# Optimization experiments

Measured on AMD Instinct MI355X. Metric: run time of the kernel, lower is better.

The kernel has to match this reference:

```python
import jax, jax.numpy as jnp
import numpy as np
from functools import partial

B, N, D = 32, 256, 1024
H = 16
HD = D // H
CD = 1024          # cond_dim
E = 4              # num_experts
TOPK = 2
DFF = 4 * D        # expert hidden
RH = 2 * D         # router mlp hidden
TEMP = 1.0
EPS = 1e-5


def _ln(x, g, b):
    mu = jnp.mean(x, axis=-1, keepdims=True)
    var = jnp.var(x, axis=-1, keepdims=True)
    return (x - mu) * jax.lax.rsqrt(var + EPS) * g + b


def setup_inputs() -> dict:
    key = jax.random.key(0)
    ks = jax.random.split(key, 16)
    s = 0.02
    return {
        "x": jax.random.normal(ks[0], (B, N, D), jnp.float32),
        "cond": jax.random.normal(ks[1], (B, 1, CD), jnp.float32),
        "ln1_g": jnp.ones((D,), jnp.float32),
        "ln1_b": jnp.zeros((D,), jnp.float32),
        "qkv_w": jax.random.normal(ks[2], (D, 3 * D), jnp.float32) * s,
        "proj_w": jax.random.normal(ks[3], (D, D), jnp.float32) * s,
        "proj_b": jnp.zeros((D,), jnp.float32),
        "ln2_g": jnp.ones((D,), jnp.float32),
        "ln2_b": jnp.zeros((D,), jnp.float32),
        "r_fc1_w": jax.random.normal(ks[4], (D + CD, RH), jnp.float32) * s,
        "r_fc1_b": jnp.zeros((RH,), jnp.float32),
        "r_fc2_w": jax.random.normal(ks[5], (RH, E), jnp.float32) * s,
        "r_fc2_b": jnp.zeros((E,), jnp.float32),
        "e_w1": jax.random.normal(ks[6], (E, D, DFF), jnp.float32) * s,
        "e_b1": jnp.zeros((E, DFF), jnp.float32),
        "e_w2": jax.random.normal(ks[7], (E, DFF, D), jnp.float32) * s,
        "e_b2": jnp.zeros((E, D), jnp.float32),
    }


def reference(x, cond, ln1_g, ln1_b, qkv_w, proj_w, proj_b, ln2_g, ln2_b,
              r_fc1_w, r_fc1_b, r_fc2_w, r_fc2_b, e_w1, e_b1, e_w2, e_b2):
    gelu = partial(jax.nn.gelu, approximate=False)  # torch nn.GELU default (erf)

    # ---- Attention block (pre-LN, no mask, qkv_bias=False) ----
    h = _ln(x, ln1_g, ln1_b)
    qkv = (h @ qkv_w).reshape(B, N, 3, H, HD)
    q, k, v = jnp.moveaxis(qkv, 2, 0)                         # each [B,N,H,HD]
    scale = HD ** -0.5
    attn = jnp.einsum("bqhd,bkhd->bhqk", q * scale, k)        # [B,H,N,N]
    attn = jax.nn.softmax(attn, axis=-1)
    o = jnp.einsum("bhqk,bkhd->bqhd", attn, v).reshape(B, N, D)
    x = x + o @ proj_w + proj_b

    # ---- RouterCond: concat tokens with repeated cond, MLP -> expert logits ----
    h = _ln(x, ln2_g, ln2_b)
    cond_rep = jnp.broadcast_to(cond, (B, N, CD))             # repeat along seq
    rin = jnp.concatenate([h, cond_rep], axis=-1).reshape(-1, D + CD)  # [T, D+CD]
    logits = gelu(rin @ r_fc1_w + r_fc1_b) @ r_fc2_w + r_fc2_b         # [T, E]
    logits = (logits - jnp.max(logits, axis=-1, keepdims=True)) / TEMP
    probs = jnp.clip(jax.nn.softmax(logits, axis=-1), 1e-9, 1.0 - 1e-9)

    # top-k selection + renormalization, scatter to dense router mask [T, E]
    top_p, top_i = jax.lax.top_k(probs, TOPK)
    top_w = top_p / jnp.sum(top_p, axis=-1, keepdims=True)    # normalize=True
    T = B * N
    router_mask = jnp.zeros((T, E), probs.dtype).at[
        jnp.arange(T)[:, None], top_i].set(top_w)             # [T, E]

    # ---- Expert MLPs, combined by router weights ----
    hf = h.reshape(T, D)
    hid = gelu(jnp.einsum("td,edh->teh", hf, e_w1) + e_b1)    # [T, E, DFF]
    eout = jnp.einsum("teh,ehd->ted", hid, e_w2) + e_b2       # [T, E, D]
    moe = jnp.einsum("te,ted->td", router_mask, eout).reshape(B, N, D)

    return x + moe
```

## Files before the change

kernel.cpp:

```cpp
#include <hip/hip_runtime.h>


typedef unsigned short u16;
typedef unsigned int   u32;

typedef __bf16 bf16x8 __attribute__((ext_vector_type(8)));
typedef float  floatx4 __attribute__((ext_vector_type(4)));

__device__ __forceinline__ float b2f(u32 u) {
    union { float f; u32 i; } v; v.i = (u & 0xffffu) << 16; return v.f;
}
__device__ __forceinline__ u16 f2b(float f) {
    union { float f; u32 i; } v; v.f = f;
    u32 x = v.i;
    u32 r = (x + 0x7fffu + ((x >> 16) & 1u)) >> 16;
    return (u16)r;
}
__device__ __forceinline__ float gelu_f(float x) {
    return 0.5f * x * (1.0f + erff(x * 0.70710678118654752440f));
}
__device__ __forceinline__ float lmix(const void* p, size_t i, int isf) {
    return isf ? ((const float*)p)[i] : b2f(((const u16*)p)[i]);
}
__device__ __forceinline__ void ld8(const void* p, size_t i, int isf, float w[8]) {
    if (isf) {
        const float* q = (const float*)p + i;
        float4 a = *(const float4*)q, b = *(const float4*)(q + 4);
        w[0] = a.x; w[1] = a.y; w[2] = a.z; w[3] = a.w;
        w[4] = b.x; w[5] = b.y; w[6] = b.z; w[7] = b.w;
    } else {
        const u16* q = (const u16*)p + i;
        uint4 r = *(const uint4*)q;
        w[0] = b2f(r.x); w[1] = b2f(r.x >> 16);
        w[2] = b2f(r.y); w[3] = b2f(r.y >> 16);
        w[4] = b2f(r.z); w[5] = b2f(r.z >> 16);
        w[6] = b2f(r.w); w[7] = b2f(r.w >> 16);
    }
}
__device__ __forceinline__ void ld4(const void* p, size_t i, int isf, float w[4]) {
    if (isf) {
        float4 a = *(const float4*)((const float*)p + i);
        w[0] = a.x; w[1] = a.y; w[2] = a.z; w[3] = a.w;
    } else {
        uint2 r = *(const uint2*)((const u16*)p + i);
        w[0] = b2f(r.x); w[1] = b2f(r.x >> 16);
        w[2] = b2f(r.y); w[3] = b2f(r.y >> 16);
    }
}

__global__ void init_kernel(const void* x0, int* cb) {
    __shared__ int sh[256];
    const int tid = threadIdx.x;
    if (tid < 12) cb[tid] = 0;
    int bad = 0;
    const u16* p = (const u16*)x0;
    for (int i = tid; i < 4096; i += 256) {
        float v = b2f(p[2 * i]);
        float a = fabsf(v);
        if (!(a <= 1e3f) || (v != 0.f && a < 1e-8f)) bad++;
    }
    sh[tid] = bad;
    __syncthreads();
    for (int s = 128; s > 0; s >>= 1) {
        if (tid < s) sh[tid] += sh[tid + s];
        __syncthreads();
    }
    if (tid == 0) cb[12] = (sh[0] > 512) ? 1 : 0;
}

__global__ __launch_bounds__(256) void cond_kernel(
    const void* __restrict__ cond, const void* __restrict__ w1,
    float* __restrict__ ct, const int* __restrict__ flg)
{
    const int isf = flg[12];
    const int b = blockIdx.y;
    const int col0 = blockIdx.x * 64;
    const int tid = threadIdx.x;
    const int wave = tid >> 6, lane = tid & 63;
    __shared__ float a[1024];
    __shared__ float part[4][64];
    {
        float v[4];
        ld4(cond, (size_t)b * 1024 + tid * 4, isf, v);
        a[tid * 4 + 0] = v[0]; a[tid * 4 + 1] = v[1];
        a[tid * 4 + 2] = v[2]; a[tid * 4 + 3] = v[3];
    }
    __syncthreads();
    const int col = col0 + lane;
    float s = 0.f;
    const int kbase = wave * 256;
    #pragma unroll 4
    for (int k = 0; k < 256; k++)
        s = fmaf(a[kbase + k], lmix(w1, (size_t)(1024 + kbase + k) * 2048 + col, isf), s);
    part[wave][lane] = s;
    __syncthreads();
    if (wave == 0) {
        float r = (part[0][lane] + part[1][lane]) + (part[2][lane] + part[3][lane]);
        ct[(size_t)b * 2048 + col] = r;
    }
}

__global__ __launch_bounds__(256) void pack_ln_kernel(
    int mode, const void* __restrict__ xin, size_t rowbase,
    const void* __restrict__ g, const void* __restrict__ bta,
    const float* __restrict__ mu_g, const float* __restrict__ rs_g,
    u16* __restrict__ hpk, u16* __restrict__ hb, const int* __restrict__ flg)
{
    const int isf = flg[12];
    const int row = blockIdx.x, tid = threadIdx.x;
    float v[4];
    float mu, rsv;
    __shared__ float red[8];
    __shared__ float mu_rs[2];
    if (mode == 0) {
        ld4(xin, (rowbase + row) * 1024 + tid * 4, isf, v);
        float s = v[0] + v[1] + v[2] + v[3];
        float q = v[0] * v[0] + v[1] * v[1] + v[2] * v[2] + v[3] * v[3];
        #pragma unroll
        for (int off = 32; off > 0; off >>= 1) {
            s += __shfl_down(s, off, 64);
            q += __shfl_down(q, off, 64);
        }
        int wid = tid >> 6, lane = tid & 63;
        if (lane == 0) { red[wid] = s; red[4 + wid] = q; }
        __syncthreads();
        if (tid == 0) {
            float ts = red[0] + red[1] + red[2] + red[3];
            float tq = red[4] + red[5] + red[6] + red[7];
            float m = ts * (1.0f / 1024.0f);
            float var = tq * (1.0f / 1024.0f) - m * m;
            float xx = var + 1e-5f;
            float r = rsqrtf(xx);
            r = r * (1.5f - 0.5f * xx * r * r);
            mu_rs[0] = m; mu_rs[1] = r;
        }
        __syncthreads();
        mu = mu_rs[0]; rsv = mu_rs[1];
    } else {
        float4 t = *(const float4*)((const float*)xin + (rowbase + row) * 1024 + tid * 4);
        v[0] = t.x; v[1] = t.y; v[2] = t.z; v[3] = t.w;
        mu = mu_g[rowbase + row]; rsv = rs_g[rowbase + row];
    }
    float gg[4], bb[4];
    ld4(g, tid * 4, isf, gg);
    ld4(bta, tid * 4, isf, bb);
    u16 hi[4], lo[4];
    #pragma unroll
    for (int i = 0; i < 4; i++) {
        float h = (v[i] - mu) * rsv * gg[i] + bb[i];
        hi[i] = f2b(h);
        lo[i] = f2b(h - b2f(hi[i]));
    }
    uint2 ph, pl;
    ph.x = (u32)hi[0] | ((u32)hi[1] << 16);
    ph.y = (u32)hi[2] | ((u32)hi[3] << 16);
    pl.x = (u32)lo[0] | ((u32)lo[1] << 16);
    pl.y = (u32)lo[2] | ((u32)lo[3] << 16);
    *(uint2*)(hpk + (size_t)row * 2048 + tid * 4) = ph;
    *(uint2*)(hpk + (size_t)row * 2048 + 1024 + tid * 4) = pl;
    if (hb) *(uint2*)(hb + (rowbase + row) * 1024 + tid * 4) = ph;
}

__global__ __launch_bounds__(256) void pack_wt_kernel(
    const void* __restrict__ W, int N, int K,
    u16* __restrict__ Bt, const int* __restrict__ flg)
{
    const int isf = flg[12];
    __shared__ float sh[64][65];
    const int k0 = blockIdx.x * 64, n0 = blockIdx.y * 64;
    const int tid = threadIdx.x;
    #pragma unroll
    for (int i = 0; i < 4; i++) {
        int r = (tid >> 4) + i * 16, c = (tid & 15) * 4;
        float w[4];
        ld4(W, (size_t)(k0 + r) * N + n0 + c, isf, w);
        sh[r][c] = w[0]; sh[r][c + 1] = w[1]; sh[r][c + 2] = w[2]; sh[r][c + 3] = w[3];
    }
    __syncthreads();
    const int n = tid >> 2, kc = (tid & 3) * 16;
    u16 hi[16], lo[16];
    #pragma unroll
    for (int j = 0; j < 16; j++) {
        float v = sh[kc + j][n];
        hi[j] = f2b(v);
        lo[j] = f2b(v - b2f(hi[j]));
    }
    u16* dst = Bt + (size_t)(n0 + n) * (2 * K) + k0 + kc;
    uint4 a, b;
    a.x = (u32)hi[0] | ((u32)hi[1] << 16);  a.y = (u32)hi[2] | ((u32)hi[3] << 16);
    a.z = (u32)hi[4] | ((u32)hi[5] << 16);  a.w = (u32)hi[6] | ((u32)hi[7] << 16);
    b.x = (u32)hi[8] | ((u32)hi[9] << 16);  b.y = (u32)hi[10] | ((u32)hi[11] << 16);
    b.z = (u32)hi[12] | ((u32)hi[13] << 16); b.w = (u32)hi[14] | ((u32)hi[15] << 16);
    *(uint4*)dst = a; *(uint4*)(dst + 8) = b;
    a.x = (u32)lo[0] | ((u32)lo[1] << 16);  a.y = (u32)lo[2] | ((u32)lo[3] << 16);
    a.z = (u32)lo[4] | ((u32)lo[5] << 16);  a.w = (u32)lo[6] | ((u32)lo[7] << 16);
    b.x = (u32)lo[8] | ((u32)lo[9] << 16);  b.y = (u32)lo[10] | ((u32)lo[11] << 16);
    b.z = (u32)lo[12] | ((u32)lo[13] << 16); b.w = (u32)lo[14] | ((u32)lo[15] << 16);
    *(uint4*)(dst + K) = a; *(uint4*)(dst + K + 8) = b;
}

__global__ __launch_bounds__(256) void pack_wtb_kernel(
    const void* __restrict__ W, size_t wOff, int N, int K,
    u16* __restrict__ Bt, const int* __restrict__ flg)
{
    const int isf = flg[12];
    __shared__ float sh[64][65];
    const int k0 = blockIdx.x * 64, n0 = blockIdx.y * 64;
    const int tid = threadIdx.x;
    #pragma unroll
    for (int i = 0; i < 4; i++) {
        int r = (tid >> 4) + i * 16, c = (tid & 15) * 4;
        float w[4];
        ld4(W, wOff + (size_t)(k0 + r) * N + n0 + c, isf, w);
        sh[r][c] = w[0]; sh[r][c + 1] = w[1]; sh[r][c + 2] = w[2]; sh[r][c + 3] = w[3];
    }
    __syncthreads();
    const int n = tid >> 2, kc = (tid & 3) * 16;
    u16 hi[16];
    #pragma unroll
    for (int j = 0; j < 16; j++) hi[j] = f2b(sh[kc + j][n]);
    u16* dst = Bt + (size_t)(n0 + n) * K + k0 + kc;
    uint4 a, b;
    a.x = (u32)hi[0] | ((u32)hi[1] << 16);  a.y = (u32)hi[2] | ((u32)hi[3] << 16);
    a.z = (u32)hi[4] | ((u32)hi[5] << 16);  a.w = (u32)hi[6] | ((u32)hi[7] << 16);
    b.x = (u32)hi[8] | ((u32)hi[9] << 16);  b.y = (u32)hi[10] | ((u32)hi[11] << 16);
    b.z = (u32)hi[12] | ((u32)hi[13] << 16); b.w = (u32)hi[14] | ((u32)hi[15] << 16);
    *(uint4*)dst = a; *(uint4*)(dst + 8) = b;
}

__global__ __launch_bounds__(256) void pack_sb_rows_kernel(
    const float* __restrict__ src, u16* __restrict__ dst)
{
    const int row = blockIdx.x, tid = threadIdx.x;
    float4 t = *(const float4*)(src + (size_t)row * 1024 + tid * 4);
    float v[4] = {t.x, t.y, t.z, t.w};
    u16 hi[4], lo[4];
    #pragma unroll
    for (int i = 0; i < 4; i++) {
        hi[i] = f2b(v[i]);
        lo[i] = f2b(v[i] - b2f(hi[i]));
    }
    uint2 ph, pl;
    ph.x = (u32)hi[0] | ((u32)hi[1] << 16);
    ph.y = (u32)hi[2] | ((u32)hi[3] << 16);
    pl.x = (u32)lo[0] | ((u32)lo[1] << 16);
    pl.y = (u32)lo[2] | ((u32)lo[3] << 16);
    *(uint2*)(dst + (size_t)row * 2048 + tid * 4) = ph;
    *(uint2*)(dst + (size_t)row * 2048 + 1024 + tid * 4) = pl;
}

#define SB_PLAIN 0
#define SB_FC1   1
#define SB_PROJ  2

__global__ __launch_bounds__(256) void gemm_sb(
    int mode,
    const u16* __restrict__ Ap,
    const u16* __restrict__ Bt,
    int K,
    float* __restrict__ C, int ldc,
    const void* __restrict__ bias,
    const float* __restrict__ condt,
    const void* __restrict__ resid,
    int rowbase, const int* __restrict__ flg)
{
    const int isf = flg[12];
    __shared__ __align__(16) u16 Ah[128][40];
    __shared__ __align__(16) u16 Al[128][40];
    __shared__ __align__(16) u16 Bh[128][40];
    __shared__ __align__(16) u16 Bl[128][40];
    const int tid = threadIdx.x;
    const int row0 = blockIdx.y * 128, col0 = blockIdx.x * 128;
    const int wave = tid >> 6, lane = tid & 63;
    const int wm = (wave >> 1) * 64, wn = (wave & 1) * 64;
    const int ln = lane & 15, quad = lane >> 4;
    const size_t K2 = (size_t)2 * K;
    floatx4 acc[4][4];
    #pragma unroll
    for (int i = 0; i < 4; i++)
        #pragma unroll
        for (int j = 0; j < 4; j++) acc[i][j] = (floatx4){0.f, 0.f, 0.f, 0.f};

    const int ar = tid >> 1, ac = (tid & 1) * 16;
    uint4 pa0, pa1, pal0, pal1, pb0, pb1, pbl0, pbl1;

    {
        const u16* ap = Ap + (size_t)(row0 + ar) * K2 + ac;
        pa0 = *(const uint4*)ap;        pa1 = *(const uint4*)(ap + 8);
        pal0 = *(const uint4*)(ap + K); pal1 = *(const uint4*)(ap + K + 8);
        const u16* bp = Bt + (size_t)(col0 + ar) * K2 + ac;
        pb0 = *(const uint4*)bp;        pb1 = *(const uint4*)(bp + 8);
        pbl0 = *(const uint4*)(bp + K); pbl1 = *(const uint4*)(bp + K + 8);
    }

    for (int k0 = 0; k0 < K; k0 += 32) {
        __syncthreads();
        *(uint4*)&Ah[ar][ac] = pa0;  *(uint4*)&Ah[ar][ac + 8] = pa1;
        *(uint4*)&Al[ar][ac] = pal0; *(uint4*)&Al[ar][ac + 8] = pal1;
        *(uint4*)&Bh[ar][ac] = pb0;  *(uint4*)&Bh[ar][ac + 8] = pb1;
        *(uint4*)&Bl[ar][ac] = pbl0; *(uint4*)&Bl[ar][ac + 8] = pbl1;
        __syncthreads();
        if (k0 + 32 < K) {
            const u16* ap = Ap + (size_t)(row0 + ar) * K2 + k0 + 32 + ac;
            pa0 = *(const uint4*)ap;        pa1 = *(const uint4*)(ap + 8);
            pal0 = *(const uint4*)(ap + K); pal1 = *(const uint4*)(ap + K + 8);
            const u16* bp = Bt + (size_t)(col0 + ar) * K2 + k0 + 32 + ac;
            pb0 = *(const uint4*)bp;        pb1 = *(const uint4*)(bp + 8);
            pbl0 = *(const uint4*)(bp + K); pbl1 = *(const uint4*)(bp + K + 8);
        }
        bf16x8 ah[4], al[4];
        #pragma unroll
        for (int mt = 0; mt < 4; mt++) {
            ah[mt] = *(const bf16x8*)&Ah[wm + mt * 16 + ln][quad * 8];
            al[mt] = *(const bf16x8*)&Al[wm + mt * 16 + ln][quad * 8];
        }
        #pragma unroll
        for (int nt = 0; nt < 4; nt++) {
            bf16x8 bh = *(const bf16x8*)&Bh[wn + nt * 16 + ln][quad * 8];
            bf16x8 bl = *(const bf16x8*)&Bl[wn + nt * 16 + ln][quad * 8];
            #pragma unroll
            for (int mt = 0; mt < 4; mt++) {
                acc[mt][nt] = __builtin_amdgcn_mfma_f32_16x16x32_bf16(ah[mt], bh, acc[mt][nt], 0, 0, 0);
                acc[mt][nt] = __builtin_amdgcn_mfma_f32_16x16x32_bf16(ah[mt], bl, acc[mt][nt], 0, 0, 0);
                acc[mt][nt] = __builtin_amdgcn_mfma_f32_16x16x32_bf16(al[mt], bh, acc[mt][nt], 0, 0, 0);
            }
        }
    }
    #pragma unroll
    for (int mt = 0; mt < 4; mt++) {
        #pragma unroll
        for (int nt = 0; nt < 4; nt++) {
            #pragma unroll
            for (int r = 0; r < 4; r++) {
                int row = row0 + wm + mt * 16 + quad * 4 + r;
                int col = col0 + wn + nt * 16 + ln;
                float v = acc[mt][nt][r];
                if (mode == SB_FC1)
                    v = gelu_f(v + lmix(bias, col, isf) +
                               condt[(size_t)((rowbase + row) >> 8) * 2048 + col]);
                else if (mode == SB_PROJ)
                    v += lmix(bias, col, isf) + lmix(resid, (size_t)row * ldc + col, isf);
                C[(size_t)row * ldc + col] = v;
            }
        }
    }
}

#define MOE_FC1 0
#define MOE_FC2 1

__global__ __launch_bounds__(256) void gemm_moe(
    int mode,
    const u16* __restrict__ Ap,
    const u16* __restrict__ Bt,
    int K,
    u16* __restrict__ C, int ldc,
    const void* __restrict__ bias, size_t biasOff,
    const float* __restrict__ rowscale,
    const int* __restrict__ toklist,
    const int* __restrict__ cb, int e, int rowOff,
    const int* __restrict__ flg)
{
    const int isf = flg[12];
    const int Meff = cb[e];
    const int gbase = cb[4 + e];
    const int rg0 = rowOff + blockIdx.y * 128;
    if (rg0 >= Meff) return;
    const int col0 = blockIdx.x * 128;
    __shared__ __align__(16) u16 As[128][40];
    __shared__ __align__(16) u16 Bs[128][40];
    const int tid = threadIdx.x;
    const int wave = tid >> 6, lane = tid & 63;
    const int wm = (wave >> 1) * 64, wn = (wave & 1) * 64;
    const int ln = lane & 15, quad = lane >> 4;
    floatx4 acc[4][4];
    #pragma unroll
    for (int i = 0; i < 4; i++)
        #pragma unroll
        for (int j = 0; j < 4; j++) acc[i][j] = (floatx4){0.f, 0.f, 0.f, 0.f};

    const int ar = tid >> 1, ac = (tid & 1) * 16;
    const int rg = rg0 + ar;
    const bool valid = (rg < Meff);
    const u16* arow;
    if (mode == MOE_FC1) {
        int tokid = valid ? toklist[gbase + rg] : 0;
        arow = Ap + (size_t)tokid * K;
    } else {
        arow = Ap + (size_t)(rg - rowOff) * K;
    }
    const u16* brow = Bt + (size_t)(col0 + ar) * K;
    uint4 pa0 = {0u,0u,0u,0u}, pa1 = {0u,0u,0u,0u}, pb0, pb1;
    if (valid) { pa0 = *(const uint4*)(arow + ac); pa1 = *(const uint4*)(arow + ac + 8); }
    pb0 = *(const uint4*)(brow + ac); pb1 = *(const uint4*)(brow + ac + 8);

    for (int k0 = 0; k0 < K; k0 += 32) {
        __syncthreads();
        *(uint4*)&As[ar][ac] = pa0; *(uint4*)&As[ar][ac + 8] = pa1;
        *(uint4*)&Bs[ar][ac] = pb0; *(uint4*)&Bs[ar][ac + 8] = pb1;
        __syncthreads();
        if (k0 + 32 < K) {
            if (valid) {
                pa0 = *(const uint4*)(arow + k0 + 32 + ac);
                pa1 = *(const uint4*)(arow + k0 + 32 + ac + 8);
            }
            pb0 = *(const uint4*)(brow + k0 + 32 + ac);
            pb1 = *(const uint4*)(brow + k0 + 32 + ac + 8);
        }
        bf16x8 a[4];
        #pragma unroll
        for (int mt = 0; mt < 4; mt++)
            a[mt] = *(const bf16x8*)&As[wm + mt * 16 + ln][quad * 8];
        #pragma unroll
        for (int nt = 0; nt < 4; nt++) {
            bf16x8 b = *(const bf16x8*)&Bs[wn + nt * 16 + ln][quad * 8];
            #pragma unroll
            for (int mt = 0; mt < 4; mt++)
                acc[mt][nt] = __builtin_amdgcn_mfma_f32_16x16x32_bf16(a[mt], b, acc[mt][nt], 0, 0, 0);
        }
    }
    #pragma unroll
    for (int mt = 0; mt < 4; mt++) {
        #pragma unroll
        for (int nt = 0; nt < 4; nt++) {
            #pragma unroll
            for (int r = 0; r < 4; r++) {
                int gw = rg0 + wm + mt * 16 + quad * 4 + r;
                if (gw >= Meff) continue;
                int col = col0 + wn + nt * 16 + ln;
                float v = acc[mt][nt][r] + lmix(bias, biasOff + col, isf);
                if (mode == MOE_FC1) {
                    C[(size_t)(gw - rowOff) * ldc + col] = f2b(gelu_f(v));
                } else {
                    v *= rowscale[gbase + gw];
                    C[(size_t)(gbase + gw) * ldc + col] = f2b(v);
                }
            }
        }
    }
}

__global__ __launch_bounds__(256) void gemm_moe2(
    const u16* __restrict__ Ap,
    const u16* __restrict__ Bt,
    u16* __restrict__ C,
    const void* __restrict__ bias, size_t biasOff,
    const float* __restrict__ rowscale,
    const int* __restrict__ cb, int e, int rowOff,
    const int* __restrict__ flg)
{
    const int isf = flg[12];
    const int Meff = cb[e];
    const int gbase = cb[4 + e];
    const int rg0 = rowOff + blockIdx.y * 128;
    if (rg0 >= Meff) return;
    const int col0 = blockIdx.x * 64;
    const int K = 4096;
    __shared__ __align__(16) u16 As[128][40];
    __shared__ __align__(16) u16 Bs[64][40];
    const int tid = threadIdx.x;
    const int wave = tid >> 6, lane = tid & 63;
    const int ln = lane & 15, quad = lane >> 4;
    floatx4 acc[2][4];
    #pragma unroll
    for (int i = 0; i < 2; i++)
        #pragma unroll
        for (int j = 0; j < 4; j++) acc[i][j] = (floatx4){0.f, 0.f, 0.f, 0.f};

    const int ar = tid >> 1, ac = (tid & 1) * 16;
    const int br = tid >> 2, bc = (tid & 3) * 8;
    const int rg = rg0 + ar;
    const bool valid = (rg < Meff);
    const u16* arow = Ap + (size_t)(rg - rowOff) * K;
    const u16* brow = Bt + (size_t)(col0 + br) * K;
    uint4 pa0 = {0u,0u,0u,0u}, pa1 = {0u,0u,0u,0u}, pb;
    if (valid) { pa0 = *(const uint4*)(arow + ac); pa1 = *(const uint4*)(arow + ac + 8); }
    pb = *(const uint4*)(brow + bc);

    for (int k0 = 0; k0 < K; k0 += 32) {
        __syncthreads();
        *(uint4*)&As[ar][ac] = pa0; *(uint4*)&As[ar][ac + 8] = pa1;
        *(uint4*)&Bs[br][bc] = pb;
        __syncthreads();
        if (k0 + 32 < K) {
            if (valid) {
                pa0 = *(const uint4*)(arow + k0 + 32 + ac);
                pa1 = *(const uint4*)(arow + k0 + 32 + ac + 8);
            }
            pb = *(const uint4*)(brow + k0 + 32 + bc);
        }
        bf16x8 a0 = *(const bf16x8*)&As[wave * 32 + ln][quad * 8];
        bf16x8 a1 = *(const bf16x8*)&As[wave * 32 + 16 + ln][quad * 8];
        #pragma unroll
        for (int nt = 0; nt < 4; nt++) {
            bf16x8 b = *(const bf16x8*)&Bs[nt * 16 + ln][quad * 8];
            acc[0][nt] = __builtin_amdgcn_mfma_f32_16x16x32_bf16(a0, b, acc[0][nt], 0, 0, 0);
            acc[1][nt] = __builtin_amdgcn_mfma_f32_16x16x32_bf16(a1, b, acc[1][nt], 0, 0, 0);
        }
// ... 364 lines not shown
    float* Ks = sh;
    float* Vs = sh + 64 * 68;

    const int q = qt * 64 + lane;
    float qreg[64];
    const float* qp = qkv + (size_t)(b * 256 + q) * 3072 + hh * 64;
    #pragma unroll
    for (int i = 0; i < 16; i++) *(float4*)&qreg[i * 4] = *(const float4*)(qp + i * 4);

    float oa[64];
    #pragma unroll
    for (int d = 0; d < 64; d++) oa[d] = 0.f;
    float m = -1e30f, l = 0.f;

    for (int s = 0; s < 4; s++) {
        __syncthreads();
        {
            int r = tid >> 2;
            int c = (tid & 3) * 16;
            int key = (r >> 4) * 64 + s * 16 + (r & 15);
            const float* kp = qkv + (size_t)(b * 256 + key) * 3072 + 1024 + hh * 64 + c;
            #pragma unroll
            for (int i = 0; i < 4; i++) {
                *(float4*)&Ks[r * 68 + c + i * 4] = *(const float4*)(kp + i * 4);
                *(float4*)&Vs[r * 68 + c + i * 4] = *(const float4*)(kp + 1024 + i * 4);
            }
        }
        __syncthreads();
        const float* Kw = Ks + wave * 16 * 68;
        const float* Vw = Vs + wave * 16 * 68;
        for (int jj = 0; jj < 16; jj++) {
            float s0 = 0.f, s1 = 0.f, s2 = 0.f, s3 = 0.f;
            #pragma unroll
            for (int d = 0; d < 64; d += 4) {
                s0 = fmaf(qreg[d + 0], Kw[jj * 68 + d + 0], s0);
                s1 = fmaf(qreg[d + 1], Kw[jj * 68 + d + 1], s1);
                s2 = fmaf(qreg[d + 2], Kw[jj * 68 + d + 2], s2);
                s3 = fmaf(qreg[d + 3], Kw[jj * 68 + d + 3], s3);
            }
            float sc = ((s0 + s1) + (s2 + s3)) * 0.125f;
            float mn = fmaxf(m, sc);
            float c = __expf(m - mn);
            float p = __expf(sc - mn);
            l = l * c + p;
            #pragma unroll
            for (int d = 0; d < 64; d++)
                oa[d] = fmaf(oa[d], c, p * Vw[jj * 68 + d]);
            m = mn;
        }
    }

    __syncthreads();
    if (wave == 1 || wave == 3) {
        float* dst = sh + (wave >> 1) * (64 * 66) + lane * 66;
        #pragma unroll
        for (int d = 0; d < 64; d++) dst[d] = oa[d];
        dst[64] = m; dst[65] = l;
    }
    __syncthreads();
    if (wave == 0 || wave == 2) {
        const float* src = sh + (wave >> 1) * (64 * 66) + lane * 66;
        float m2 = src[64], l2 = src[65];
        float M = fmaxf(m, m2);
        float c1 = __expf(m - M), c2 = __expf(m2 - M);
        l = l * c1 + l2 * c2;
        #pragma unroll
        for (int d = 0; d < 64; d++) oa[d] = oa[d] * c1 + src[d] * c2;
        m = M;
    }
    __syncthreads();
    if (wave == 2) {
        float* dst = sh + lane * 66;
        #pragma unroll
        for (int d = 0; d < 64; d++) dst[d] = oa[d];
        dst[64] = m; dst[65] = l;
    }
    __syncthreads();
    if (wave == 0) {
        const float* src = sh + lane * 66;
        float m2 = src[64], l2 = src[65];
        float M = fmaxf(m, m2);
        float c1 = __expf(m - M), c2 = __expf(m2 - M);
        l = l * c1 + l2 * c2;
        #pragma unroll
        for (int d = 0; d < 64; d++) oa[d] = oa[d] * c1 + src[d] * c2;
        float inv = 1.0f / l;
        float* op = o + (size_t)(b * 256 + q) * 1024 + hh * 64;
        #pragma unroll
        for (int i = 0; i < 16; i++) {
            float4 v = { oa[i * 4] * inv, oa[i * 4 + 1] * inv,
                         oa[i * 4 + 2] * inv, oa[i * 4 + 3] * inv };
            *(float4*)(op + i * 4) = v;
        }
    }
}

__global__ __launch_bounds__(256) void router_kernel(
    const float* __restrict__ hr, const void* __restrict__ w2,
    const void* __restrict__ b2, int* __restrict__ t2i,
    float* __restrict__ t2w, int* __restrict__ cb, int rowbase,
    const int* __restrict__ flg)
{
    const int isf = flg[12];
    const int lt = blockIdx.x * 4 + (threadIdx.x >> 6);
    const int t = rowbase + lt;
    const int lane = threadIdx.x & 63;
    float a0 = 0.f, a1 = 0.f, a2 = 0.f, a3 = 0.f;
    const float* hp = hr + (size_t)lt * 2048;
    #pragma unroll
    for (int it = 0; it < 8; it++) {
        const int j = it * 256 + lane * 4;
        float4 hv = *(const float4*)(hp + j);
        float w[4];
        ld4(w2, (size_t)(j + 0) * 4, isf, w);
        a0 = fmaf(hv.x, w[0], a0); a1 = fmaf(hv.x, w[1], a1);
        a2 = fmaf(hv.x, w[2], a2); a3 = fmaf(hv.x, w[3], a3);
        ld4(w2, (size_t)(j + 1) * 4, isf, w);
        a0 = fmaf(hv.y, w[0], a0); a1 = fmaf(hv.y, w[1], a1);
        a2 = fmaf(hv.y, w[2], a2); a3 = fmaf(hv.y, w[3], a3);
        ld4(w2, (size_t)(j + 2) * 4, isf, w);
        a0 = fmaf(hv.z, w[0], a0); a1 = fmaf(hv.z, w[1], a1);
        a2 = fmaf(hv.z, w[2], a2); a3 = fmaf(hv.z, w[3], a3);
        ld4(w2, (size_t)(j + 3) * 4, isf, w);
        a0 = fmaf(hv.w, w[0], a0); a1 = fmaf(hv.w, w[1], a1);
        a2 = fmaf(hv.w, w[2], a2); a3 = fmaf(hv.w, w[3], a3);
    }
    #pragma unroll
    for (int off = 32; off > 0; off >>= 1) {
        a0 += __shfl_down(a0, off, 64);
        a1 += __shfl_down(a1, off, 64);
        a2 += __shfl_down(a2, off, 64);
        a3 += __shfl_down(a3, off, 64);
    }
    if (lane == 0) {
        float l[4];
        l[0] = a0 + lmix(b2, 0, isf); l[1] = a1 + lmix(b2, 1, isf);
        l[2] = a2 + lmix(b2, 2, isf); l[3] = a3 + lmix(b2, 3, isf);
        int i0 = 0;
        #pragma unroll
        for (int i = 1; i < 4; i++) if (l[i] > l[i0]) i0 = i;
        int i1 = (i0 == 0) ? 1 : 0;
        #pragma unroll
        for (int i = 0; i < 4; i++) if (i != i0 && l[i] > l[i1]) i1 = i;
        float mx = fmaxf(fmaxf(l[0], l[1]), fmaxf(l[2], l[3]));
        float e0 = __expf(l[0] - mx), e1 = __expf(l[1] - mx);
        float e2 = __expf(l[2] - mx), e3 = __expf(l[3] - mx);
        float inv = 1.0f / (e0 + e1 + e2 + e3);
        float p[4] = { e0 * inv, e1 * inv, e2 * inv, e3 * inv };
        float b0 = fminf(fmaxf(p[i0], 1e-9f), 1.0f - 1e-9f);
        float b1 = fminf(fmaxf(p[i1], 1e-9f), 1.0f - 1e-9f);
        float winv = 1.0f / (b0 + b1);
        t2i[2 * t] = i0; t2i[2 * t + 1] = i1;
        t2w[2 * t] = b0 * winv; t2w[2 * t + 1] = b1 * winv;
        atomicAdd(&cb[i0], 1);
        atomicAdd(&cb[i1], 1);
    }
}

__global__ __launch_bounds__(256) void fill2_kernel(
    const int* __restrict__ t2i, const float* __restrict__ t2w,
    int* __restrict__ cb, int* __restrict__ tok,
    float* __restrict__ aw, int* __restrict__ apos)
{
    const int e = blockIdx.x;
    const int tid = threadIdx.x;
    __shared__ int scan[256];
    int base = 0;
    #pragma unroll
    for (int i = 0; i < 4; i++) if (i < e) base += cb[i];
    const int t0 = tid * 32;
    int cnt = 0;
    for (int t = t0; t < t0 + 32; t++)
        cnt += (t2i[2 * t] == e) + (t2i[2 * t + 1] == e);
    scan[tid] = cnt;
    __syncthreads();
    for (int off = 1; off < 256; off <<= 1) {
        int add = (tid >= off) ? scan[tid - off] : 0;
        __syncthreads();
        scan[tid] += add;
        __syncthreads();
    }
    int pos = base + scan[tid] - cnt;
    for (int t = t0; t < t0 + 32; t++) {
        #pragma unroll
        for (int j = 0; j < 2; j++) {
            if (t2i[2 * t + j] == e) {
                tok[pos] = t;
                aw[pos] = t2w[2 * t + j];
                apos[2 * t + j] = pos;
                pos++;
            }
        }
    }
    if (tid == 0) cb[4 + e] = base;
}

#define EM_FC1 0
#define EM_FC2 1

__global__ __launch_bounds__(256) void gemm_mfma(
    int mode,
    const float* __restrict__ x1,
    const float* __restrict__ mu, const float* __restrict__ rs,
    const void* __restrict__ lng, const void* __restrict__ lnb,
    const u16* __restrict__ Ab,
    const void* __restrict__ B, size_t bOff, int ldb, int K,
    u16* __restrict__ C, int ldc,
    const void* __restrict__ bias, size_t biasOff,
    const float* __restrict__ rowscale,
    const int* __restrict__ toklist,
    const int* __restrict__ cb, int e, int rowOff,
    const int* __restrict__ flg)
{
    const int isf = flg[12];
    const int Meff = cb[e];
    const int gbase = cb[4 + e];
    const int rg0 = rowOff + blockIdx.y * 64;
    if (rg0 >= Meff) return;
    const int col0 = blockIdx.x * 64;
    __shared__ __align__(16) u16 As[64][72];
    __shared__ __align__(16) u16 Bs[64][72];
    const int tid = threadIdx.x;
    const int wave = tid >> 6, lane = tid & 63;
    const int ln = lane & 15, quad = lane >> 4;
    floatx4 acc[4];
    #pragma unroll
    for (int nt = 0; nt < 4; nt++) acc[nt] = (floatx4){0.f, 0.f, 0.f, 0.f};

    const int ar = tid >> 2, ac = (tid & 3) * 8;
    const int bk = tid >> 3, bn = (tid & 7) * 8;
    const int rg = rg0 + ar;
    const bool valid = (rg < Meff);
    int tokid = 0; float lm = 0.f, lr = 0.f;
    if (mode == EM_FC1 && valid) {
        tokid = toklist[gbase + rg];
        lm = mu[tokid]; lr = rs[tokid];
    }

    for (int k0 = 0; k0 < K; k0 += 32) {
        __syncthreads();
        if (mode == EM_FC1) {
            uint4 packed = {0u, 0u, 0u, 0u};
            if (valid) {
                float4 p0 = *(const float4*)(x1 + (size_t)tokid * 1024 + k0 + ac);
                float4 p1 = *(const float4*)(x1 + (size_t)tokid * 1024 + k0 + ac + 4);
                float pv[8] = {p0.x, p0.y, p0.z, p0.w, p1.x, p1.y, p1.z, p1.w};
                float gg[8], bb[8];
                ld8(lng, k0 + ac, isf, gg);
                ld8(lnb, k0 + ac, isf, bb);
                u16 wb[8];
                #pragma unroll
                for (int z = 0; z < 8; z++)
                    wb[z] = f2b((pv[z] - lm) * lr * gg[z] + bb[z]);
                packed.x = (u32)wb[0] | ((u32)wb[1] << 16);
                packed.y = (u32)wb[2] | ((u32)wb[3] << 16);
                packed.z = (u32)wb[4] | ((u32)wb[5] << 16);
                packed.w = (u32)wb[6] | ((u32)wb[7] << 16);
            }
            *(uint4*)&As[ar][ac] = packed;
        } else {
            uint4 av = {0u, 0u, 0u, 0u};
            if (valid) av = *(const uint4*)(Ab + (size_t)(rg - rowOff) * K + k0 + ac);
            *(uint4*)&As[ar][ac] = av;
        }
        u16 u[8];
        {
            float w[8];
            ld8(B, bOff + (size_t)(k0 + bk) * ldb + col0 + bn, isf, w);
            #pragma unroll
            for (int z = 0; z < 8; z++) u[z] = f2b(w[z]);
        }
        #pragma unroll
        for (int jj = 0; jj < 8; jj++) {
            int j = (jj + (tid & 7)) & 7;
            Bs[bn + j][bk] = u[j];
        }
        __syncthreads();
        bf16x8 af = *(const bf16x8*)&As[wave * 16 + ln][quad * 8];
        #pragma unroll
        for (int nt = 0; nt < 4; nt++) {
            bf16x8 bf = *(const bf16x8*)&Bs[nt * 16 + ln][quad * 8];
            acc[nt] = __builtin_amdgcn_mfma_f32_16x16x32_bf16(af, bf, acc[nt], 0, 0, 0);
        }
    }
    #pragma unroll
    for (int nt = 0; nt < 4; nt++) {
        #pragma unroll
        for (int r = 0; r < 4; r++) {
            int gw = rg0 + wave * 16 + quad * 4 + r;
            if (gw >= Meff) continue;
            int gcol = col0 + nt * 16 + ln;
            float v = acc[nt][r] + lmix(bias, biasOff + gcol, isf);
            if (mode == EM_FC1) {
                C[(size_t)(gw - rowOff) * ldc + gcol] = f2b(gelu_f(v));
            } else {
                v *= rowscale[gbase + gw];
                C[(size_t)(gbase + gw) * ldc + gcol] = f2b(v);
            }
        }
    }
}

__global__ __launch_bounds__(256) void combine_kernel(
    const float* __restrict__ x1, const u16* __restrict__ eo,
    const int* __restrict__ apos, void* __restrict__ outv,
    const int* __restrict__ flg)
{
    const int isf = flg[12];
    int t = blockIdx.x;
    int c = threadIdx.x * 4;
    int p0 = apos[2 * t], p1 = apos[2 * t + 1];
    float4 xv = *(const float4*)(x1 + (size_t)t * 1024 + c);
    uint2 ea = *(const uint2*)(eo + (size_t)p0 * 1024 + c);
    uint2 eb = *(const uint2*)(eo + (size_t)p1 * 1024 + c);
    float r0 = xv.x + b2f(ea.x) + b2f(eb.x);
    float r1 = xv.y + b2f(ea.x >> 16) + b2f(eb.x >> 16);
    float r2 = xv.z + b2f(ea.y) + b2f(eb.y);
    float r3 = xv.w + b2f(ea.y >> 16) + b2f(eb.y >> 16);
    if (isf) {
        float4 res = {r0, r1, r2, r3};
        *(float4*)((float*)outv + (size_t)t * 1024 + c) = res;
    } else {
        uint2 res;
        res.x = (u32)f2b(r0) | ((u32)f2b(r1) << 16);
        res.y = (u32)f2b(r2) | ((u32)f2b(r3) << 16);
        *(uint2*)((u16*)outv + (size_t)t * 1024 + c) = res;
    }
}

extern "C" void kernel_launch(void* const* d_in, const int* in_sizes, int n_in,
                              void* d_out, int out_size, void* d_ws, size_t ws_size,
                              hipStream_t stream)
{
    const void* x      = d_in[0];
    const void* cond   = d_in[1];
    const void* ln1_g  = d_in[2];
    const void* ln1_b  = d_in[3];
    const void* qkv_w  = d_in[4];
    const void* proj_w = d_in[5];
    const void* proj_b = d_in[6];
    const void* ln2_g  = d_in[7];
    const void* ln2_b  = d_in[8];
    const void* rf1w   = d_in[9];
    const void* rf1b   = d_in[10];
    const void* rf2w   = d_in[11];
    const void* rf2b   = d_in[12];
    const void* ew1    = d_in[13];
    const void* eb1    = d_in[14];
    const void* ew2    = d_in[15];
    const void* eb2    = d_in[16];
    (void)in_sizes; (void)n_in; (void)out_size;

    char* ws = (char*)d_ws;
    const size_t MB = 1024 * 1024;
    const bool fat = ws_size >= (size_t)116 * MB;

    float* x1   = (float*)(ws);
    u16*   qkvt = (u16*)(ws);
    u16*   hpk  = (u16*)(ws + 12 * MB);
    float* qkvcFb = (float*)(ws + 16 * MB);
    char*  B1   = ws + 32 * MB;
    float* ob   = (float*)B1;
    u16*   rf1tF= (u16*)B1;
    u16*   h2tF = (u16*)(ws + 40 * MB);
    u16*   eo   = (u16*)B1;
    u16*   rf1tB= (u16*)B1;
    char*  R    = ws + 64 * MB;
    float* qkvcF= (float*)R;
    u16*   h2tB = (u16*)R;
    float* hrcB = (float*)(R + 8 * MB);
    float* hrcF = (float*)R;
    u16*   hid  = (u16*)R;
    u16*   obp  = (u16*)R;
    u16*   ew1t = (u16*)(R + 16 * MB);
    u16*   ew2t = (u16*)(R + 24 * MB);
    u16*   pwt  = (u16*)(ws + 96 * MB);
    u16*   h2b  = (u16*)(ws + 96 * MB);
    char*  ST   = ws + (fat ? 112 : 96) * MB;

    size_t so = 0;
    auto salloc = [&](size_t bytes) { size_t o = so; so += (bytes + 255) & ~(size_t)255; return o; };
    float* mu   = (float*)(ST + salloc(8192 * 4));
    float* rs   = (float*)(ST + salloc(8192 * 4));
    float* ct   = (float*)(ST + salloc((size_t)32 * 2048 * 4));
    int*   t2i  = (int*)  (ST + salloc(16384 * 4));
    float* t2w  = (float*)(ST + salloc(16384 * 4));
    int*   cb   = (int*)  (ST + salloc(16 * 4));
    int*   tok  = (int*)  (ST + salloc(16384 * 4));
    float* aw   = (float*)(ST + salloc(16384 * 4));
    int*   apos = (int*)  (ST + salloc(16384 * 4));

    init_kernel<<<1, 256, 0, stream>>>(x, cb);

    pack_wt_kernel<<<dim3(16, 48), 256, 0, stream>>>(qkv_w, 3072, 1024, qkvt, cb);
    if (fat) {
        for (int c = 0; c < 2; c++) {
            const size_t r0 = (size_t)c * 4096;
            pack_ln_kernel<<<4096, 256, 0, stream>>>(
                0, x, r0, ln1_g, ln1_b, nullptr, nullptr, hpk, nullptr, cb);
            gemm_sb<<<dim3(24, 32), 256, 0, stream>>>(
                SB_PLAIN, hpk, qkvt, 1024, qkvcF, 3072, nullptr, nullptr, nullptr, 0, cb);
            attn_mfma_kernel<<<1024, 256, 0, stream>>>(qkvcF, ob + r0 * 1024);
        }
    } else {
        for (int c = 0; c < 8; c++) {
            const size_t r0 = (size_t)c * 1024;
            pack_ln_kernel<<<1024, 256, 0, stream>>>(
                0, x, r0, ln1_g, ln1_b, nullptr, nullptr, hpk, nullptr, cb);
            gemm_sb<<<dim3(24, 8), 256, 0, stream>>>(
                SB_PLAIN, hpk, qkvt, 1024, qkvcFb, 3072, nullptr, nullptr, nullptr, 0, cb);
            attn_kernel<<<256, 256, 0, stream>>>(qkvcFb, ob + r0 * 1024);
        }
    }

    if (fat) {
        pack_sb_rows_kernel<<<8192, 256, 0, stream>>>(ob, obp);
        pack_wt_kernel<<<dim3(16, 16), 256, 0, stream>>>(proj_w, 1024, 1024, pwt, cb);
        gemm_sb<<<dim3(8, 64), 256, 0, stream>>>(
            SB_PROJ, obp, pwt, 1024, x1, 1024, proj_b, nullptr, x, 0, cb);
    } else {
        gemm_f32<<<dim3(8, 64), 256, 0, stream>>>(
            GM_PROJ, 0, (const void*)ob, 1024, proj_w, 1024, 0, 8192, 1024, 1024,
            x1, 1024, proj_b, x, cb);
    }

    ln_stats_kernel<<<8192, 256, 0, stream>>>(x1, mu, rs);

    cond_kernel<<<dim3(32, 32), 256, 0, stream>>>(cond, rf1w, ct, cb);

    if (fat) {
        pack_wt_kernel<<<dim3(16, 32), 256, 0, stream>>>(rf1w, 2048, 1024, rf1tF, cb);
        for (int rc = 0; rc < 2; rc++) {
            const int rb = rc * 4096;
            pack_ln_kernel<<<4096, 256, 0, stream>>>(
                1, x1, rb, ln2_g, ln2_b, mu, rs, h2tF, h2b, cb);
            gemm_sb<<<dim3(16, 32), 256, 0, stream>>>(
                SB_FC1, h2tF, rf1tF, 1024, hrcF, 2048, rf1b, ct, nullptr, rb, cb);
            router_kernel<<<1024, 256, 0, stream>>>(hrcF, rf2w, rf2b, t2i, t2w, cb, rb, cb);
        }
    } else {
        pack_wt_kernel<<<dim3(16, 32), 256, 0, stream>>>(rf1w, 2048, 1024, rf1tB, cb);
        for (int rc = 0; rc < 4; rc++) {
            const int rb = rc * 2048;
            pack_ln_kernel<<<2048, 256, 0, stream>>>(
                1, x1, rb, ln2_g, ln2_b, mu, rs, h2tB, nullptr, cb);
            gemm_sb<<<dim3(16, 16), 256, 0, stream>>>(
                SB_FC1, h2tB, rf1tB, 1024, hrcB, 2048, rf1b, ct, nullptr, rb, cb);
            router_kernel<<<512, 256, 0, stream>>>(hrcB, rf2w, rf2b, t2i, t2w, cb, rb, cb);
        }
    }
    fill2_kernel<<<4, 256, 0, stream>>>(t2i, t2w, cb, tok, aw, apos);

    if (fat) {
        for (int e = 0; e < 4; e++) {
            pack_wtb_kernel<<<dim3(16, 64), 256, 0, stream>>>(
                ew1, (size_t)e * 1024 * 4096, 4096, 1024, ew1t, cb);
            pack_wtb_kernel<<<dim3(64, 16), 256, 0, stream>>>(
                ew2, (size_t)e * 4096 * 1024, 1024, 4096, ew2t, cb);
            for (int c = 0; c < 4; c++) {
                const int ro = c * 2048;
                gemm_moe<<<dim3(32, 16), 256, 0, stream>>>(
                    MOE_FC1, h2b, ew1t, 1024, hid, 4096,
                    eb1, (size_t)e * 4096, nullptr, tok, cb, e, ro, cb);
                gemm_moe2<<<dim3(16, 16), 256, 0, stream>>>(
                    hid, ew2t, eo, eb2, (size_t)e * 1024, aw, cb, e, ro, cb);
            }
        }
    } else {
        for (int e = 0; e < 4; e++) {
            for (int c = 0; c < 2; c++) {
                const int ro = c * 4096;
                gemm_mfma<<<dim3(64, 64), 256, 0, stream>>>(
                    EM_FC1, x1, mu, rs, ln2_g, ln2_b, nullptr,
                    ew1, (size_t)e * 1024 * 4096, 4096, 1024,
                    hid, 4096, eb1, (size_t)e * 4096, nullptr, tok, cb, e, ro, cb);
                gemm_mfma<<<dim3(16, 64), 256, 0, stream>>>(
                    EM_FC2, nullptr, nullptr, nullptr, nullptr, nullptr, hid,
                    ew2, (size_t)e * 4096 * 1024, 1024, 4096,
                    eo, 1024, eb2, (size_t)e * 1024, aw, tok, cb, e, ro, cb);
            }
        }
    }

    combine_kernel<<<8192, 256, 0, stream>>>(x1, eo, apos, d_out, cb);
}
```

Baseline: 2.021 ms.

## Fuse router fc2 projection into fc1 GEMM epilogue with atomic logit accumulation

The router fc1 GEMM epilogue now applies GELU, multiplies by the fc2 weights, reduces across lanes with shuffles and atomically adds partial logits into a small [T,4] buffer. This avoids writing and re-reading the [rows,2048] fp32 hidden activation. A separate top2 kernel then does softmax and top-2, and fill2 derives per-expert counts from a 4-way scan instead of global atomics. The cost is float atomics, whose summation order is nondeterministic, plus extra zeroing and top2 launches.

New measurement: 1.908 ms. 5.6% less time.

```diff
diff --git a/kernel.cpp b/kernel.cpp
--- a/kernel.cpp
+++ b/kernel.cpp
@@ -68,6 +68,10 @@
     if (tid == 0) cb[12] = (sh[0] > 512) ? 1 : 0;
 }
 
+__global__ __launch_bounds__(256) void zero_lg_kernel(float* __restrict__ lg) {
+    lg[blockIdx.x * 256 + threadIdx.x] = 0.f;
+}
+
 __global__ __launch_bounds__(256) void cond_kernel(
     const void* __restrict__ cond, const void* __restrict__ w1,
     float* __restrict__ ct, const int* __restrict__ flg)
@@ -262,6 +266,8 @@
     const void* __restrict__ bias,
     const float* __restrict__ condt,
     const void* __restrict__ resid,
+    const void* __restrict__ w2,
+    float* __restrict__ lg,
     int rowbase, const int* __restrict__ flg)
 {
     const int isf = flg[12];
@@ -326,24 +332,89 @@
             }
         }
     }
-    #pragma unroll
-    for (int mt = 0; mt < 4; mt++) {
-        #pragma unroll
-        for (int nt = 0; nt < 4; nt++) {
+    if (mode == SB_FC1) {
+        float w2r[4][4];
+        #pragma unroll
+        for (int nt = 0; nt < 4; nt++)
+            ld4(w2, (size_t)(col0 + wn + nt * 16 + ln) * 4, isf, w2r[nt]);
+        #pragma unroll
+        for (int mt = 0; mt < 4; mt++) {
             #pragma unroll
             for (int r = 0; r < 4; r++) {
                 int row = row0 + wm + mt * 16 + quad * 4 + r;
-                int col = col0 + wn + nt * 16 + ln;
-                float v = acc[mt][nt][r];
-                if (mode == SB_FC1)
-                    v = gelu_f(v + lmix(bias, col, isf) +
-                               condt[(size_t)((rowbase + row) >> 8) * 2048 + col]);
-                else if (mode == SB_PROJ)
-                    v += lmix(bias, col, isf) + lmix(resid, (size_t)row * ldc + col, isf);
-                C[(size_t)row * ldc + col] = v;
-            }
-        }
-    }
+                float p0 = 0.f, p1 = 0.f, p2 = 0.f, p3 = 0.f;
+                #pragma unroll
+                for (int nt = 0; nt < 4; nt++) {
+                    int col = col0 + wn + nt * 16 + ln;
+                    float v = gelu_f(acc[mt][nt][r] + lmix(bias, col, isf) +
+                                     condt[(size_t)((rowbase + row) >> 8) * 2048 + col]);
+                    p0 = fmaf(v, w2r[nt][0], p0);
+                    p1 = fmaf(v, w2r[nt][1], p1);
+                    p2 = fmaf(v, w2r[nt][2], p2);
+                    p3 = fmaf(v, w2r[nt][3], p3);
+                }
+                #pragma unroll
+                for (int off = 1; off < 16; off <<= 1) {
+                    p0 += __shfl_xor(p0, off, 16);
+                    p1 += __shfl_xor(p1, off, 16);
+                    p2 += __shfl_xor(p2, off, 16);
+                    p3 += __shfl_xor(p3, off, 16);
+                }
+                if (ln == 0) {
+                    float* dst = lg + (size_t)(rowbase + row) * 4;
+                    atomicAdd(dst + 0, p0);
+                    atomicAdd(dst + 1, p1);
+                    atomicAdd(dst + 2, p2);
+                    atomicAdd(dst + 3, p3);
+                }
+            }
+        }
+    } else {
+        #pragma unroll
+        for (int mt = 0; mt < 4; mt++) {
+            #pragma unroll
+            for (int nt = 0; nt < 4; nt++) {
+                #pragma unroll
+                for (int r = 0; r < 4; r++) {
+                    int row = row0 + wm + mt * 16 + quad * 4 + r;
+                    int col = col0 + wn + nt * 16 + ln;
+                    float v = acc[mt][nt][r];
+                    if (mode == SB_PROJ)
+                        v += lmix(bias, col, isf) + lmix(resid, (size_t)row * ldc + col, isf);
+                    C[(size_t)row * ldc + col] = v;
+                }
+            }
+        }
+    }
+}
+
+__global__ __launch_bounds__(256) void top2_kernel(
+    const float* __restrict__ lg, const void* __restrict__ b2,
+    int* __restrict__ t2i, float* __restrict__ t2w,
+    const int* __restrict__ flg)
+{
+    const int isf = flg[12];
+    const int t = blockIdx.x * 256 + threadIdx.x;
+    float l[4];
+    #pragma unroll
+    for (int i = 0; i < 4; i++)
+        l[i] = lg[(size_t)t * 4 + i] + lmix(b2, i, isf);
+    int i0 = 0;
+    #pragma unroll
+    for (int i = 1; i < 4; i++) if (l[i] > l[i0]) i0 = i;
+    int i1 = (i0 == 0) ? 1 : 0;
+    #pragma unroll
+    for (int i = 0; i < 4; i++) if (i != i0 && l[i] > l[i1]) i1 = i;
+    float mx = fmaxf(fmaxf(l[0], l[1]), fmaxf(l[2], l[3]));
+    float e0 = __expf(l[0] - mx), e1 = __expf(l[1] - mx);
+    float e2 = __expf(l[2] - mx), e3 = __expf(l[3] - mx);
+    float inv = 1.0f / (e0 + e1 + e2 + e3);
+    float p[4] = { e0 * inv, e1 * inv, e2 * inv, e3 * inv };
+    float b0 = fminf(fmaxf(p[i0], 1e-9f), 1.0f - 1e-9f);
+    float b1 = fminf(fmaxf(p[i1], 1e-9f), 1.0f - 1e-9f);
+    float winv = 1.0f / (b0 + b1);
+    t2i[2 * t] = i0; t2i[2 * t + 1] = i1;
+    t2w[2 * t] = b0 * winv; t2w[2 * t + 1] = b1 * winv;
 }
 
 #define MOE_FC1 0
@@ -1014,8 +1085,6 @@
         float winv = 1.0f / (b0 + b1);
         t2i[2 * t] = i0; t2i[2 * t + 1] = i1;
         t2w[2 * t] = b0 * winv; t2w[2 * t + 1] = b1 * winv;
-        atomicAdd(&cb[i0], 1);
-        atomicAdd(&cb[i1], 1);
     }
 }
 
@@ -1026,23 +1095,30 @@
 {
     const int e = blockIdx.x;
     const int tid = threadIdx.x;
-    __shared__ int scan[256];
-    int base = 0;
-    #pragma unroll
-    for (int i = 0; i < 4; i++) if (i < e) base += cb[i];
+    __shared__ int scan4[4][256];
     const int t0 = tid * 32;
-    int cnt = 0;
-    for (int t = t0; t < t0 + 32; t++)
-        cnt += (t2i[2 * t] == e) + (t2i[2 * t + 1] == e);
-    scan[tid] = cnt;
+    int cnt[4] = {0, 0, 0, 0};
+    for (int t = t0; t < t0 + 32; t++) {
+        cnt[t2i[2 * t]]++;
+        cnt[t2i[2 * t + 1]]++;
+    }
+    #pragma unroll
+    for (int k = 0; k < 4; k++) scan4[k][tid] = cnt[k];
     __syncthreads();
     for (int off = 1; off < 256; off <<= 1) {
-        int add = (tid >= off) ? scan[tid - off] : 0;
-        __syncthreads();
-        scan[tid] += add;
-        __syncthreads();
-    }
-    int pos = base + scan[tid] - cnt;
+        int add[4];
+        #pragma unroll
+        for (int k = 0; k < 4; k++)
+            add[k] = (tid >= off) ? scan4[k][tid - off] : 0;
+        __syncthreads();
+        #pragma unroll
+        for (int k = 0; k < 4; k++) scan4[k][tid] += add[k];
+        __syncthreads();
+    }
+    int base = 0;
+    #pragma unroll
+    for (int k = 0; k < 4; k++) if (k < e) base += scan4[k][255];
+    int pos = base + scan4[e][tid] - cnt[e];
     for (int t = t0; t < t0 + 32; t++) {
         #pragma unroll
         for (int j = 0; j < 2; j++) {
@@ -1054,7 +1130,7 @@
             }
         }
     }
-    if (tid == 0) cb[4 + e] = base;
+    if (tid == 0) { cb[e] = scan4[e][255]; cb[4 + e] = base; }
 }
 
 #define EM_FC1 0
@@ -1231,7 +1307,6 @@
     float* qkvcF= (float*)R;
     u16*   h2tB = (u16*)R;
     float* hrcB = (float*)(R + 8 * MB);
-    float* hrcF = (float*)R;
     u16*   hid  = (u16*)R;
     u16*   obp  = (u16*)R;
     u16*   ew1t = (u16*)(R + 16 * MB);
@@ -1251,6 +1326,7 @@
     int*   tok  = (int*)  (ST + salloc(16384 * 4));
     float* aw   = (float*)(ST + salloc(16384 * 4));
     int*   apos = (int*)  (ST + salloc(16384 * 4));
+    float* lg   = (float*)(ST + salloc(32768 * 4));
 
     init_kernel<<<1, 256, 0, stream>>>(x, cb);
 
@@ -1261,7 +1337,8 @@
             pack_ln_kernel<<<4096, 256, 0, stream>>>(
                 0, x, r0, ln1_g, ln1_b, nullptr, nullptr, hpk, nullptr, cb);
             gemm_sb<<<dim3(24, 32), 256, 0, stream>>>(
-                SB_PLAIN, hpk, qkvt, 1024, qkvcF, 3072, nullptr, nullptr, nullptr, 0, cb);
+                SB_PLAIN, hpk, qkvt, 1024, qkvcF, 3072, nullptr, nullptr, nullptr,
+                nullptr, nullptr, 0, cb);
             attn_mfma_kernel<<<1024, 256, 0, stream>>>(qkvcF, ob + r0 * 1024);
         }
     } else {
@@ -1270,7 +1347,8 @@
             pack_ln_kernel<<<1024, 256, 0, stream>>>(
                 0, x, r0, ln1_g, ln1_b, nullptr, nullptr, hpk, nullptr, cb);
             gemm_sb<<<dim3(24, 8), 256, 0, stream>>>(
-                SB_PLAIN, hpk, qkvt, 1024, qkvcFb, 3072, nullptr, nullptr, nullptr, 0, cb);
+                SB_PLAIN, hpk, qkvt, 1024, qkvcFb, 3072, nullptr, nullptr, nullptr,
+                nullptr, nullptr, 0, cb);
             attn_kernel<<<256, 256, 0, stream>>>(qkvcFb, ob + r0 * 1024);
         }
     }
@@ -1279,7 +1357,8 @@
         pack_sb_rows_kernel<<<8192, 256, 0, stream>>>(ob, obp);
         pack_wt_kernel<<<dim3(16, 16), 256, 0, stream>>>(proj_w, 1024, 1024, pwt, cb);
         gemm_sb<<<dim3(8, 64), 256, 0, stream>>>(
-            SB_PROJ, obp, pwt, 1024, x1, 1024, proj_b, nullptr, x, 0, cb);
+            SB_PROJ, obp, pwt, 1024, x1, 1024, proj_b, nullptr, x,
+            nullptr, nullptr, 0, cb);
     } else {
         gemm_f32<<<dim3(8, 64), 256, 0, stream>>>(
             GM_PROJ, 0, (const void*)ob, 1024, proj_w, 1024, 0, 8192, 1024, 1024,
@@ -1291,25 +1370,29 @@
     cond_kernel<<<dim3(32, 32), 256, 0, stream>>>(cond, rf1w, ct, cb);
 
     if (fat) {
+        zero_lg_kernel<<<128, 256, 0, stream>>>(lg);
         pack_wt_kernel<<<dim3(16, 32), 256, 0, stream>>>(rf1w, 2048, 1024, rf1tF, cb);
         for (int rc = 0; rc < 2; rc++) {
             const int rb = rc * 4096;
             pack_ln_kernel<<<4096, 256, 0, stream>>>(
                 1, x1, rb, ln2_g, ln2_b, mu, rs, h2tF, h2b, cb);
             gemm_sb<<<dim3(16, 32), 256, 0, stream>>>(
-                SB_FC1, h2tF, rf1tF, 1024, hrcF, 2048, rf1b, ct, nullptr, rb, cb);
-            router_kernel<<<1024, 256, 0, stream>>>(hrcF, rf2w, rf2b, t2i, t2w, cb, rb, cb);
-        }
+                SB_FC1, h2tF, rf1tF, 1024, nullptr, 2048, rf1b, ct, nullptr,
+                rf2w, lg, rb, cb);
+        }
+        top2_kernel<<<32, 256, 0, stream>>>(lg, rf2b, t2i, t2w, cb);
     } else {
         pack_wt_kernel<<<dim3(16, 32), 256, 0, stream>>>(rf1w, 2048, 1024, rf1tB, cb);
+        zero_lg_kernel<<<128, 256, 0, stream>>>(lg);
         for (int rc = 0; rc < 4; rc++) {
             const int rb = rc * 2048;
             pack_ln_kernel<<<2048, 256, 0, stream>>>(
                 1, x1, rb, ln2_g, ln2_b, mu, rs, h2tB, nullptr, cb);
             gemm_sb<<<dim3(16, 16), 256, 0, stream>>>(
-                SB_FC1, h2tB, rf1tB, 1024, hrcB, 2048, rf1b, ct, nullptr, rb, cb);
-            router_kernel<<<512, 256, 0, stream>>>(hrcB, rf2w, rf2b, t2i, t2w, cb, rb, cb);
-        }
+                SB_FC1, h2tB, rf1tB, 1024, nullptr, 2048, rf1b, ct, nullptr,
+                rf2w, lg, rb, cb);
+        }
+        top2_kernel<<<32, 256, 0, stream>>>(lg, rf2b, t2i, t2w, cb);
     }
     fill2_kernel<<<4, 256, 0, stream>>>(t2i, t2w, cb, tok, aw, apos);
 
```
